# Optimization experiments

Measured on AMD Instinct MI355X. Metric: run time of the kernel, lower is better.

The kernel has to match this reference:

```python
import jax, jax.numpy as jnp
import numpy as np

POOL_RAD = 1.0   # init kwarg pool_rad
N = 16384        # total points
B = 8            # graphs in batch
F = 128          # feature dim
BIG = 1e30

def _voxel_keys(pos, batch, rad):
    # torch_geometric.voxel_grid with start=min-rad/2, end=max+rad/2, batch as extra dim
    start = pos.min(0) - rad * 0.5
    end = pos.max(0) + rad * 0.5
    nv = jnp.floor((end - start) / rad).astype(jnp.int32) + 1  # voxels per spatial dim
    c = jnp.floor((pos - start) / rad).astype(jnp.int32)       # [N,3] voxel coords
    lin = c[:, 0] + c[:, 1] * nv[0] + c[:, 2] * nv[0] * nv[1]
    return lin + batch.astype(jnp.int32) * (nv[0] * nv[1] * nv[2])

def _consecutive(keys, n):
    # consecutive_cluster: relabel to sorted-consecutive ids; perm = last index per cluster
    _, inv = jnp.unique(keys, return_inverse=True, size=n,
                        fill_value=jnp.iinfo(jnp.int32).max)
    inv = inv.reshape(-1)
    perm = jax.ops.segment_max(jnp.arange(n, dtype=jnp.int32), inv, num_segments=n)
    counts = jax.ops.segment_sum(jnp.ones((n,), jnp.int32), inv, num_segments=n)
    return inv, jnp.clip(perm, 0, n - 1), counts

def _nearest(pos, batch, cpos, cbatch, cvalid):
    # nearest centroid within the same graph; invalid/padded centroids masked out
    d = (pos * pos).sum(1)[:, None] - 2.0 * (pos @ cpos.T) + (cpos * cpos).sum(1)[None, :]
    ok = (batch[:, None] == cbatch[None, :]) & cvalid[None, :]
    return jnp.argmin(jnp.where(ok, d, BIG), axis=1)

def _pool(pos, x, batch):
    n = pos.shape[0]
    # stage 1: voxel-grid clustering, centroid positions
    inv1, perm1, cnt1 = _consecutive(_voxel_keys(pos, batch, POOL_RAD), n)
    c1 = jnp.maximum(cnt1, 1).astype(pos.dtype)[:, None]
    cpos = jax.ops.segment_sum(pos, inv1, num_segments=n) / c1
    cbatch = batch[perm1]
    # stage 2: reassign each point to its nearest voxel centroid, relabel
    cl2 = _nearest(jax.lax.stop_gradient(pos), batch,
                   jax.lax.stop_gradient(cpos), cbatch, cnt1 > 0)
    inv2, perm2, cnt2 = _consecutive(cl2, n)
    valid2 = cnt2 > 0
    c2 = jnp.maximum(cnt2, 1).astype(pos.dtype)[:, None]
    pos_out = jax.ops.segment_sum(pos, inv2, num_segments=n) / c2   # mean pos
    x_out = jax.ops.segment_max(x, inv2, num_segments=n)            # aggr='max'
    x_out = jnp.where(valid2[:, None], x_out, 0.0)
    pos_out = jnp.where(valid2[:, None], pos_out, 0.0)
    batch_out = jnp.where(valid2, batch[perm2], -1)
    return x_out, pos_out, batch_out

def setup_inputs():
    key = jax.random.key(0)
    k1, k2 = jax.random.split(key)
    pos = jax.random.uniform(k1, (N, 3), jnp.float32) * 10.0
    x = jax.random.normal(k2, (N, F), jnp.float32)
    batch = jnp.repeat(jnp.arange(B, dtype=jnp.int32), N // B)
    return {"pos": pos, "x": x, "batch": batch}

def reference(pos, x, batch):
    return _pool(pos, x, batch)
```

## Files before the change

kernel.cpp:

```cpp
#include <hip/hip_runtime.h>

#define TPB 256
#define K1SZ 32768

static __device__ __forceinline__ unsigned int fmap(float f) {
  unsigned int b = __float_as_uint(f);
  return (b & 0x80000000u) ? ~b : (b | 0x80000000u);
}
static __device__ __forceinline__ float funmap(unsigned int u) {
  unsigned int b = (u & 0x80000000u) ? (u & 0x7fffffffu) : ~u;
  return __uint_as_float(b);
}

static __device__ __forceinline__ int wave_incl_scan(int v, int lane) {
  #pragma unroll
  for (int off = 1; off < 64; off <<= 1) {
    int u = __shfl_up(v, off);
    if (lane >= off) v += u;
  }
  return v;
}

__global__ void k_init(double* __restrict__ sum1, double* __restrict__ sum2,
                       int* __restrict__ cnt1, int* __restrict__ cnt2,
                       int* __restrict__ perm2, int* __restrict__ flags1,
                       int* __restrict__ flags2, unsigned int* __restrict__ xacc,
                       const float* __restrict__ pos, float* __restrict__ scal,
                       int n, int F) {
  int t = blockIdx.x * blockDim.x + threadIdx.x;
  if (t < n * F) xacc[t] = 0u;
  if (t < 3 * n) { sum1[t] = 0.0; sum2[t] = 0.0; }
  if (t < n) { cnt1[t] = 0; cnt2[t] = 0; perm2[t] = -1; flags2[t] = 0; }
  if (t < K1SZ) flags1[t] = 0;

  if (blockIdx.x == 0) {
    const int tid = threadIdx.x;
    const int lane = tid & 63, wid = tid >> 6;
    float mn[3] = {3.4e38f, 3.4e38f, 3.4e38f};
    float mx[3] = {-3.4e38f, -3.4e38f, -3.4e38f};
    const float4* p4 = (const float4*)pos;
    int np4 = n >> 2;
    for (int j = tid; j < np4; j += TPB) {
      float4 a = p4[3 * j], b = p4[3 * j + 1], c = p4[3 * j + 2];
      mn[0] = fminf(mn[0], fminf(fminf(a.x, a.w), fminf(b.z, c.y)));
      mx[0] = fmaxf(mx[0], fmaxf(fmaxf(a.x, a.w), fmaxf(b.z, c.y)));
      mn[1] = fminf(mn[1], fminf(fminf(a.y, b.x), fminf(b.w, c.z)));
      mx[1] = fmaxf(mx[1], fmaxf(fmaxf(a.y, b.x), fmaxf(b.w, c.z)));
      mn[2] = fminf(mn[2], fminf(fminf(a.z, b.y), fminf(c.x, c.w)));
      mx[2] = fmaxf(mx[2], fmaxf(fmaxf(a.z, b.y), fmaxf(c.x, c.w)));
    }
    if (tid == 0) {
      for (int i = np4 * 4; i < n; ++i)
        for (int d = 0; d < 3; ++d) {
          float v = pos[i * 3 + d];
          mn[d] = fminf(mn[d], v);
          mx[d] = fmaxf(mx[d], v);
        }
    }
    #pragma unroll
    for (int off = 32; off > 0; off >>= 1) {
      #pragma unroll
      for (int d = 0; d < 3; ++d) {
        mn[d] = fminf(mn[d], __shfl_xor(mn[d], off));
        mx[d] = fmaxf(mx[d], __shfl_xor(mx[d], off));
      }
    }
    __shared__ float smn[4][3], smx[4][3];
    if (lane == 0)
      for (int d = 0; d < 3; ++d) { smn[wid][d] = mn[d]; smx[wid][d] = mx[d]; }
    __syncthreads();
    if (tid == 0) {
      float rmn[3], rmx[3];
      for (int d = 0; d < 3; ++d) { rmn[d] = smn[0][d]; rmx[d] = smx[0][d]; }
      for (int w = 1; w < 4; ++w)
        for (int d = 0; d < 3; ++d) {
          rmn[d] = fminf(rmn[d], smn[w][d]);
          rmx[d] = fmaxf(rmx[d], smx[w][d]);
        }
      int nv[3];
      for (int d = 0; d < 3; ++d) {
        float start = rmn[d] - 0.5f;
        float end   = rmx[d] + 0.5f;
        nv[d] = (int)floorf(end - start) + 1;
        scal[d] = start;
      }
      int* isc = (int*)(scal + 3);
      isc[0] = nv[0];
      isc[1] = nv[0] * nv[1];
      isc[2] = nv[0] * nv[1] * nv[2];
      isc[3] = nv[1];
      isc[4] = nv[2];
    }
  }
}

__global__ void k_keys(const float* __restrict__ pos, const int* __restrict__ batch, int n,
                       const float* __restrict__ scal, int* __restrict__ key1,
                       int* __restrict__ flags1) {
  int i = blockIdx.x * blockDim.x + threadIdx.x;
  if (i >= n) return;
  const int* isc = (const int*)(scal + 3);
  int c0 = (int)floorf(pos[i * 3 + 0] - scal[0]);
  int c1 = (int)floorf(pos[i * 3 + 1] - scal[1]);
  int c2 = (int)floorf(pos[i * 3 + 2] - scal[2]);
  int key = c0 + c1 * isc[0] + c2 * isc[1] + batch[i] * isc[2];
  key = min(max(key, 0), K1SZ - 1);
  key1[i] = key;
  flags1[key] = 1;
}

__global__ __launch_bounds__(1024) void k_scan(const int* __restrict__ flags,
                                               int* __restrict__ rank, int L) {
  const int t = threadIdx.x;
  const int lane = t & 63;
  const int wid = t >> 6;
  __shared__ int wsum[16];
  const int4* f4 = (const int4*)flags;
  int4* r4 = (int4*)rank;
  const int n4 = L >> 2;
  int base = 0;
  for (int tile = 0; tile * 1024 < n4; ++tile) {
    int i = tile * 1024 + t;
    int4 v = (i < n4) ? f4[i] : int4{0, 0, 0, 0};
    int q0 = v.x, q1 = q0 + v.y, q2 = q1 + v.z, q3 = q2 + v.w;
    int ws = wave_incl_scan(q3, lane);
    if (lane == 63) wsum[wid] = ws;
    __syncthreads();
    int woff = 0, ttot = 0;
    #pragma unroll
    for (int w = 0; w < 16; ++w) {
      int s = wsum[w];
      if (w < wid) woff += s;
      ttot += s;
    }
    int e = base + woff + (ws - q3);
    if (i < n4) r4[i] = int4{e, e + q0, e + q1, e + q2};
    base += ttot;
    __syncthreads();
  }
}

__global__ void k_assign1(const float* __restrict__ pos, int n,
                          const int* __restrict__ key1, const int* __restrict__ rank1,
                          int* __restrict__ cnt1, double* __restrict__ sum1) {
  int i = blockIdx.x * blockDim.x + threadIdx.x;
  if (i >= n) return;
  int c = rank1[key1[i]];
  atomicAdd(&cnt1[c], 1);
  atomicAdd(&sum1[c * 3 + 0], (double)pos[i * 3 + 0]);
  atomicAdd(&sum1[c * 3 + 1], (double)pos[i * 3 + 1]);
  atomicAdd(&sum1[c * 3 + 2], (double)pos[i * 3 + 2]);
}

__global__ void k_centroid1(int n, const int* __restrict__ cnt1, double* __restrict__ sum1) {
  int k = blockIdx.x * blockDim.x + threadIdx.x;
  if (k >= n) return;
  int c = cnt1[k];
  if (c <= 0) return;
  double inv = 1.0 / (double)c;
  sum1[k * 3 + 0] *= inv;
  sum1[k * 3 + 1] *= inv;
  sum1[k * 3 + 2] *= inv;
}

__global__ void k_nearest(const float* __restrict__ pos, const int* __restrict__ batch, int n,
                          const double* __restrict__ cpos, const int* __restrict__ flags1,
                          const int* __restrict__ rank1, const float* __restrict__ scal,
                          int* __restrict__ cl2, int* __restrict__ flags2) {
  int i = blockIdx.x * blockDim.x + threadIdx.x;
  if (i >= n) return;
  const int* isc = (const int*)(scal + 3);
  const float s0 = scal[0], s1 = scal[1], s2 = scal[2];
  const int nv0 = isc[0], nv01 = isc[1], nvtot = isc[2];
  const int nv1 = isc[3], nv2 = isc[4];
  float pxf = pos[i * 3 + 0], pyf = pos[i * 3 + 1], pzf = pos[i * 3 + 2];
  double px = pxf, py = pyf, pz = pzf;
  int c0 = (int)floorf(pxf - s0);
  int c1 = (int)floorf(pyf - s1);
  int c2 = (int)floorf(pzf - s2);
  int base = batch[i] * nvtot;
  int k0 = min(max(c0 + c1 * nv0 + c2 * nv01 + base, 0), K1SZ - 1);
  int bid = rank1[k0];
  double dx = px - cpos[bid * 3 + 0];
  double dy = py - cpos[bid * 3 + 1];
  double dz = pz - cpos[bid * 3 + 2];
  double best2 = dx * dx + dy * dy + dz * dz;
  for (int oz = -2; oz <= 2; ++oz) {
    int z = c2 + oz;
    if (z < 0 || z >= nv2) continue;
    double lz = (double)s2 + z;
    double gz = fmax(0.0, fmax(lz - pz, pz - (lz + 1.0)));
    double gz2 = gz * gz;
    if (gz2 > best2 + 1e-4) continue;
    for (int oy = -2; oy <= 2; ++oy) {
      int y = c1 + oy;
      if (y < 0 || y >= nv1) continue;
      double ly = (double)s1 + y;
      double gy = fmax(0.0, fmax(ly - py, py - (ly + 1.0)));
      double gzy2 = gz2 + gy * gy;
      if (gzy2 > best2 + 1e-4) continue;
      for (int ox = -2; ox <= 2; ++ox) {
        int xq = c0 + ox;
        if (xq < 0 || xq >= nv0) continue;
        if ((ox | oy | oz) == 0) continue;
        double lx = (double)s0 + xq;
        double gx = fmax(0.0, fmax(lx - px, px - (lx + 1.0)));
        double mind2 = gzy2 + gx * gx;
        if (mind2 > best2 + 1e-4) continue;
        int key = min(xq + y * nv0 + z * nv01 + base, K1SZ - 1);
        if (!flags1[key]) continue;
        int c = rank1[key];
        double ddx = px - cpos[c * 3 + 0];
        double ddy = py - cpos[c * 3 + 1];
        double ddz = pz - cpos[c * 3 + 2];
        double d2 = ddx * ddx + ddy * ddy + ddz * ddz;
        if (d2 < best2 || (d2 == best2 && c < bid)) { best2 = d2; bid = c; }
      }
    }
  }
  cl2[i] = bid;
  flags2[bid] = 1;
}

__global__ void k_assign2_xmax(const float* __restrict__ pos, const float* __restrict__ x,
                               int n, int F, const int* __restrict__ cl2,
                               const int* __restrict__ rank2, int* __restrict__ cnt2,
                               int* __restrict__ perm2, double* __restrict__ sum2,
                               unsigned int* __restrict__ xacc) {
  int t = blockIdx.x * blockDim.x + threadIdx.x;
  if (t >= n * F) return;
  int i = t / F;
  int f = t - i * F;
  int c = rank2[cl2[i]];
  atomicMax(&xacc[c * F + f], fmap(x[t]));
  if (f == 0) {
    atomicAdd(&cnt2[c], 1);
    atomicMax(&perm2[c], i);
    atomicAdd(&sum2[c * 3 + 0], (double)pos[i * 3 + 0]);
    atomicAdd(&sum2[c * 3 + 1], (double)pos[i * 3 + 1]);
    atomicAdd(&sum2[c * 3 + 2], (double)pos[i * 3 + 2]);
  }
}

__global__ void k_finalize(int n, int F, const int* __restrict__ cnt2,
                           const int* __restrict__ perm2, const int* __restrict__ batch,
                           const double* __restrict__ sum2, unsigned int* __restrict__ xacc,
                           float* __restrict__ pos_out, float* __restrict__ batch_out) {
  int t = blockIdx.x * blockDim.x + threadIdx.x;
  if (t < n * F) {
    int j = t / F;
    float out = 0.0f;
    if (cnt2[j] > 0) out = funmap(xacc[t]);
    ((float*)xacc)[t] = out;
  }
  if (t < n) {
    int c = cnt2[t];
    if (c > 0) {
      double inv = 1.0 / (double)c;
      pos_out[t * 3 + 0] = (float)(sum2[t * 3 + 0] * inv);
      pos_out[t * 3 + 1] = (float)(sum2[t * 3 + 1] * inv);
      pos_out[t * 3 + 2] = (float)(sum2[t * 3 + 2] * inv);
      batch_out[t] = (float)batch[perm2[t]];
    } else {
      pos_out[t * 3 + 0] = 0.0f;
      pos_out[t * 3 + 1] = 0.0f;
      pos_out[t * 3 + 2] = 0.0f;
      batch_out[t] = -1.0f;
    }
  }
}

extern "C" void kernel_launch(void* const* d_in, const int* in_sizes, int n_in,
                              void* d_out, int out_size, void* d_ws, size_t ws_size,
                              hipStream_t stream) {
  const float* pos   = (const float*)d_in[0];
  const float* x     = (const float*)d_in[1];
  const int*   batch = (const int*)d_in[2];
  int n = in_sizes[2];
  int F = in_sizes[1] / n;

  char* ws = (char*)d_ws;
  size_t off = 0;
  auto alloc = [&](size_t bytes, size_t align) -> void* {
    off = (off + align - 1) & ~(align - 1);
    void* p = ws + off;
    off += bytes;
    return p;
  };
  double* sum1   = (double*)alloc((size_t)n * 3 * sizeof(double), 16);
  double* sum2   = (double*)alloc((size_t)n * 3 * sizeof(double), 16);
  int* key1      = (int*)alloc((size_t)n * 4, 16);
  int* cl2       = (int*)alloc((size_t)n * 4, 16);
  int* cnt1      = (int*)alloc((size_t)n * 4, 16);
  int* cnt2      = (int*)alloc((size_t)n * 4, 16);
  int* perm2     = (int*)alloc((size_t)n * 4, 16);
  int* flags1    = (int*)alloc((size_t)K1SZ * 4, 16);
  int* rank1     = (int*)alloc((size_t)K1SZ * 4, 16);
  int* flags2    = (int*)alloc((size_t)n * 4, 16);
  int* rank2     = (int*)alloc((size_t)n * 4, 16);
  float* scal    = (float*)alloc(64, 16);

  unsigned int* xacc = (unsigned int*)d_out;
  float* pos_out     = (float*)d_out + (size_t)n * F;
  float* batch_out   = pos_out + (size_t)n * 3;

  int nb  = (n + TPB - 1) / TPB;
  int nbF = (n * F + TPB - 1) / TPB;
  int nbP = (n + 63) / 64;

  k_init<<<nbF, TPB, 0, stream>>>(sum1, sum2, cnt1, cnt2, perm2,
                                  flags1, flags2, xacc, pos, scal, n, F);
  k_keys<<<nb, TPB, 0, stream>>>(pos, batch, n, scal, key1, flags1);
  k_scan<<<1, 1024, 0, stream>>>(flags1, rank1, K1SZ);
  k_assign1<<<nb, TPB, 0, stream>>>(pos, n, key1, rank1, cnt1, sum1);
  k_centroid1<<<nb, TPB, 0, stream>>>(n, cnt1, sum1);
  k_nearest<<<nbP, 64, 0, stream>>>(pos, batch, n, sum1, flags1, rank1, scal, cl2, flags2);
  k_scan<<<1, 1024, 0, stream>>>(flags2, rank2, n);
  k_assign2_xmax<<<nbF, TPB, 0, stream>>>(pos, x, n, F, cl2, rank2, cnt2, perm2,
                                          sum2, xacc);
  k_finalize<<<nbF, TPB, 0, stream>>>(n, F, cnt2, perm2, batch, sum2, xacc,
                                      pos_out, batch_out);
}
```

Measured before the change: 67.15 us.

## Bound scans by active range, fold centroid divide into nearest, vectorize feature passes

The init kernel now also finds the maximum batch id, so the first scan only walks the occupied part of the key space. That scan records the total cluster count, which then bounds how many tiles the second scan processes. The separate centroid-normalisation kernel is removed; k_nearest divides the sums by the counts on the fly. Init, the x max-aggregation and finalize move to float4/uint4 accesses with four atomics per thread. The cost is extra divisions inside the neighbour search, and unwritten rank entries beyond the active range, which are assumed never to be read.

```diff
diff --git a/kernel.cpp b/kernel.cpp
--- a/kernel.cpp
+++ b/kernel.cpp
@@ -24,11 +24,11 @@
 __global__ void k_init(double* __restrict__ sum1, double* __restrict__ sum2,
                        int* __restrict__ cnt1, int* __restrict__ cnt2,
                        int* __restrict__ perm2, int* __restrict__ flags1,
-                       int* __restrict__ flags2, unsigned int* __restrict__ xacc,
-                       const float* __restrict__ pos, float* __restrict__ scal,
-                       int n, int F) {
+                       int* __restrict__ flags2, uint4* __restrict__ xacc4,
+                       const float* __restrict__ pos, const int* __restrict__ batch,
+                       float* __restrict__ scal, int n, int nF4) {
   int t = blockIdx.x * blockDim.x + threadIdx.x;
-  if (t < n * F) xacc[t] = 0u;
+  if (t < nF4) xacc4[t] = uint4{0u, 0u, 0u, 0u};
   if (t < 3 * n) { sum1[t] = 0.0; sum2[t] = 0.0; }
   if (t < n) { cnt1[t] = 0; cnt2[t] = 0; perm2[t] = -1; flags2[t] = 0; }
   if (t < K1SZ) flags1[t] = 0;
@@ -38,7 +38,9 @@
     const int lane = tid & 63, wid = tid >> 6;
     float mn[3] = {3.4e38f, 3.4e38f, 3.4e38f};
     float mx[3] = {-3.4e38f, -3.4e38f, -3.4e38f};
+    int mb = 0;
     const float4* p4 = (const float4*)pos;
+    const int4* b4 = (const int4*)batch;
     int np4 = n >> 2;
     for (int j = tid; j < np4; j += TPB) {
       float4 a = p4[3 * j], b = p4[3 * j + 1], c = p4[3 * j + 2];
@@ -48,14 +50,18 @@
       mx[1] = fmaxf(mx[1], fmaxf(fmaxf(a.y, b.x), fmaxf(b.w, c.z)));
       mn[2] = fminf(mn[2], fminf(fminf(a.z, b.y), fminf(c.x, c.w)));
       mx[2] = fmaxf(mx[2], fmaxf(fmaxf(a.z, b.y), fmaxf(c.x, c.w)));
+      int4 bb = b4[j];
+      mb = max(mb, max(max(bb.x, bb.y), max(bb.z, bb.w)));
     }
     if (tid == 0) {
-      for (int i = np4 * 4; i < n; ++i)
+      for (int i = np4 * 4; i < n; ++i) {
         for (int d = 0; d < 3; ++d) {
           float v = pos[i * 3 + d];
           mn[d] = fminf(mn[d], v);
           mx[d] = fmaxf(mx[d], v);
         }
+        mb = max(mb, batch[i]);
+      }
     }
     #pragma unroll
     for (int off = 32; off > 0; off >>= 1) {
@@ -64,19 +70,26 @@
         mn[d] = fminf(mn[d], __shfl_xor(mn[d], off));
         mx[d] = fmaxf(mx[d], __shfl_xor(mx[d], off));
       }
+      mb = max(mb, __shfl_xor(mb, off));
     }
     __shared__ float smn[4][3], smx[4][3];
-    if (lane == 0)
+    __shared__ int smb[4];
+    if (lane == 0) {
       for (int d = 0; d < 3; ++d) { smn[wid][d] = mn[d]; smx[wid][d] = mx[d]; }
+      smb[wid] = mb;
+    }
     __syncthreads();
     if (tid == 0) {
       float rmn[3], rmx[3];
+      int rmb = smb[0];
       for (int d = 0; d < 3; ++d) { rmn[d] = smn[0][d]; rmx[d] = smx[0][d]; }
-      for (int w = 1; w < 4; ++w)
+      for (int w = 1; w < 4; ++w) {
         for (int d = 0; d < 3; ++d) {
           rmn[d] = fminf(rmn[d], smn[w][d]);
           rmx[d] = fmaxf(rmx[d], smx[w][d]);
         }
+        rmb = max(rmb, smb[w]);
+      }
       int nv[3];
       for (int d = 0; d < 3; ++d) {
         float start = rmn[d] - 0.5f;
@@ -90,6 +103,7 @@
       isc[2] = nv[0] * nv[1] * nv[2];
       isc[3] = nv[1];
       isc[4] = nv[2];
+      isc[5] = rmb + 1;
     }
   }
 }
@@ -109,19 +123,18 @@
   flags1[key] = 1;
 }
 
-__global__ __launch_bounds__(1024) void k_scan(const int* __restrict__ flags,
-                                               int* __restrict__ rank, int L) {
+static __device__ __forceinline__ int scan_body(const int* __restrict__ flags,
+                                                int* __restrict__ rank,
+                                                int ntiles, int n4full, int* wsum) {
   const int t = threadIdx.x;
   const int lane = t & 63;
   const int wid = t >> 6;
-  __shared__ int wsum[16];
   const int4* f4 = (const int4*)flags;
   int4* r4 = (int4*)rank;
-  const int n4 = L >> 2;
   int base = 0;
-  for (int tile = 0; tile * 1024 < n4; ++tile) {
+  for (int tile = 0; tile < ntiles; ++tile) {
     int i = tile * 1024 + t;
-    int4 v = (i < n4) ? f4[i] : int4{0, 0, 0, 0};
+    int4 v = (i < n4full) ? f4[i] : int4{0, 0, 0, 0};
     int q0 = v.x, q1 = q0 + v.y, q2 = q1 + v.z, q3 = q2 + v.w;
     int ws = wave_incl_scan(q3, lane);
     if (lane == 63) wsum[wid] = ws;
@@ -134,10 +147,32 @@
       ttot += s;
     }
     int e = base + woff + (ws - q3);
-    if (i < n4) r4[i] = int4{e, e + q0, e + q1, e + q2};
+    if (i < n4full) r4[i] = int4{e, e + q0, e + q1, e + q2};
     base += ttot;
     __syncthreads();
   }
+  return base;
+}
+
+__global__ __launch_bounds__(1024) void k_scan1(const int* __restrict__ flags,
+                                                int* __restrict__ rank,
+                                                const float* __restrict__ scal) {
+  __shared__ int wsum[16];
+  const int* isc = (const int*)(scal + 3);
+  long long L = (long long)isc[5] * isc[2];
+  int L_eff = (int)(L > K1SZ ? K1SZ : L);
+  int ntiles = (L_eff + 4095) >> 12;
+  int base = scan_body(flags, rank, ntiles, K1SZ >> 2, wsum);
+  if (threadIdx.x == 0) rank[K1SZ] = base;
+}
+
+__global__ __launch_bounds__(1024) void k_scan2(const int* __restrict__ flags,
+                                                int* __restrict__ rank,
+                                                const int* __restrict__ total1, int n) {
+  __shared__ int wsum[16];
+  int L_eff = min(n, *total1);
+  int ntiles = (L_eff + 4095) >> 12;
+  scan_body(flags, rank, ntiles, n >> 2, wsum);
 }
 
 __global__ void k_assign1(const float* __restrict__ pos, int n,
@@ -152,20 +187,10 @@
   atomicAdd(&sum1[c * 3 + 2], (double)pos[i * 3 + 2]);
 }
 
-__global__ void k_centroid1(int n, const int* __restrict__ cnt1, double* __restrict__ sum1) {
-  int k = blockIdx.x * blockDim.x + threadIdx.x;
-  if (k >= n) return;
-  int c = cnt1[k];
-  if (c <= 0) return;
-  double inv = 1.0 / (double)c;
-  sum1[k * 3 + 0] *= inv;
-  sum1[k * 3 + 1] *= inv;
-  sum1[k * 3 + 2] *= inv;
-}
-
 __global__ void k_nearest(const float* __restrict__ pos, const int* __restrict__ batch, int n,
-                          const double* __restrict__ cpos, const int* __restrict__ flags1,
-                          const int* __restrict__ rank1, const float* __restrict__ scal,
+                          const double* __restrict__ sum1, const int* __restrict__ cnt1,
+                          const int* __restrict__ flags1, const int* __restrict__ rank1,
+                          const float* __restrict__ scal,
                           int* __restrict__ cl2, int* __restrict__ flags2) {
   int i = blockIdx.x * blockDim.x + threadIdx.x;
   if (i >= n) return;
@@ -181,40 +206,45 @@
   int base = batch[i] * nvtot;
   int k0 = min(max(c0 + c1 * nv0 + c2 * nv01 + base, 0), K1SZ - 1);
   int bid = rank1[k0];
-  double dx = px - cpos[bid * 3 + 0];
-  double dy = py - cpos[bid * 3 + 1];
-  double dz = pz - cpos[bid * 3 + 2];
-  double best2 = dx * dx + dy * dy + dz * dz;
-  for (int oz = -2; oz <= 2; ++oz) {
-    int z = c2 + oz;
-    if (z < 0 || z >= nv2) continue;
-    double lz = (double)s2 + z;
-    double gz = fmax(0.0, fmax(lz - pz, pz - (lz + 1.0)));
-    double gz2 = gz * gz;
-    if (gz2 > best2 + 1e-4) continue;
-    for (int oy = -2; oy <= 2; ++oy) {
-      int y = c1 + oy;
-      if (y < 0 || y >= nv1) continue;
-      double ly = (double)s1 + y;
-      double gy = fmax(0.0, fmax(ly - py, py - (ly + 1.0)));
-      double gzy2 = gz2 + gy * gy;
-      if (gzy2 > best2 + 1e-4) continue;
-      for (int ox = -2; ox <= 2; ++ox) {
-        int xq = c0 + ox;
-        if (xq < 0 || xq >= nv0) continue;
-        if ((ox | oy | oz) == 0) continue;
-        double lx = (double)s0 + xq;
-        double gx = fmax(0.0, fmax(lx - px, px - (lx + 1.0)));
-        double mind2 = gzy2 + gx * gx;
-        if (mind2 > best2 + 1e-4) continue;
-        int key = min(xq + y * nv0 + z * nv01 + base, K1SZ - 1);
-        if (!flags1[key]) continue;
-        int c = rank1[key];
-        double ddx = px - cpos[c * 3 + 0];
-        double ddy = py - cpos[c * 3 + 1];
-        double ddz = pz - cpos[c * 3 + 2];
-        double d2 = ddx * ddx + ddy * ddy + ddz * ddz;
-        if (d2 < best2 || (d2 == best2 && c < bid)) { best2 = d2; bid = c; }
+  {
+    double inv = 1.0 / (double)cnt1[bid];
+    double dx = px - sum1[bid * 3 + 0] * inv;
+    double dy = py - sum1[bid * 3 + 1] * inv;
+    double dz = pz - sum1[bid * 3 + 2] * inv;
+    double d2 = dx * dx + dy * dy + dz * dz;
+    double best2 = d2;
+    for (int oz = -2; oz <= 2; ++oz) {
+      int z = c2 + oz;
+      if (z < 0 || z >= nv2) continue;
+      double lz = (double)s2 + z;
+      double gz = fmax(0.0, fmax(lz - pz, pz - (lz + 1.0)));
+      double gz2 = gz * gz;
+      if (gz2 > best2 + 1e-4) continue;
+      for (int oy = -2; oy <= 2; ++oy) {
+        int y = c1 + oy;
+        if (y < 0 || y >= nv1) continue;
+        double ly = (double)s1 + y;
+        double gy = fmax(0.0, fmax(ly - py, py - (ly + 1.0)));
+        double gzy2 = gz2 + gy * gy;
+        if (gzy2 > best2 + 1e-4) continue;
+        for (int ox = -2; ox <= 2; ++ox) {
+          int xq = c0 + ox;
+          if (xq < 0 || xq >= nv0) continue;
+          if ((ox | oy | oz) == 0) continue;
+          double lx = (double)s0 + xq;
+          double gx = fmax(0.0, fmax(lx - px, px - (lx + 1.0)));
+          double mind2 = gzy2 + gx * gx;
+          if (mind2 > best2 + 1e-4) continue;
+          int key = min(xq + y * nv0 + z * nv01 + base, K1SZ - 1);
+          if (!flags1[key]) continue;
+          int c = rank1[key];
+          double cinv = 1.0 / (double)cnt1[c];
+          double ddx = px - sum1[c * 3 + 0] * cinv;
+          double ddy = py - sum1[c * 3 + 1] * cinv;
+          double ddz = pz - sum1[c * 3 + 2] * cinv;
+          double dd2 = ddx * ddx + ddy * ddy + ddz * ddz;
+          if (dd2 < best2 || (dd2 == best2 && c < bid)) { best2 = dd2; bid = c; }
+        }
       }
     }
   }
@@ -222,18 +252,23 @@
   flags2[bid] = 1;
 }
 
-__global__ void k_assign2_xmax(const float* __restrict__ pos, const float* __restrict__ x,
-                               int n, int F, const int* __restrict__ cl2,
+__global__ void k_assign2_xmax(const float* __restrict__ pos, const float4* __restrict__ x4,
+                               int n, int F4, int F, const int* __restrict__ cl2,
                                const int* __restrict__ rank2, int* __restrict__ cnt2,
                                int* __restrict__ perm2, double* __restrict__ sum2,
                                unsigned int* __restrict__ xacc) {
   int t = blockIdx.x * blockDim.x + threadIdx.x;
-  if (t >= n * F) return;
-  int i = t / F;
-  int f = t - i * F;
+  if (t >= n * F4) return;
+  int i = t / F4;
+  int q = t - i * F4;
   int c = rank2[cl2[i]];
-  atomicMax(&xacc[c * F + f], fmap(x[t]));
-  if (f == 0) {
+  float4 v = x4[t];
+  unsigned int* dst = &xacc[c * F + q * 4];
+  atomicMax(dst + 0, fmap(v.x));
+  atomicMax(dst + 1, fmap(v.y));
+  atomicMax(dst + 2, fmap(v.z));
+  atomicMax(dst + 3, fmap(v.w));
+  if (q == 0) {
     atomicAdd(&cnt2[c], 1);
     atomicMax(&perm2[c], i);
     atomicAdd(&sum2[c * 3 + 0], (double)pos[i * 3 + 0]);
@@ -242,16 +277,19 @@
   }
 }
 
-__global__ void k_finalize(int n, int F, const int* __restrict__ cnt2,
+__global__ void k_finalize(int n, int F4, const int* __restrict__ cnt2,
                            const int* __restrict__ perm2, const int* __restrict__ batch,
-                           const double* __restrict__ sum2, unsigned int* __restrict__ xacc,
+                           const double* __restrict__ sum2, uint4* __restrict__ xacc4,
                            float* __restrict__ pos_out, float* __restrict__ batch_out) {
   int t = blockIdx.x * blockDim.x + threadIdx.x;
-  if (t < n * F) {
-    int j = t / F;
-    float out = 0.0f;
-    if (cnt2[j] > 0) out = funmap(xacc[t]);
-    ((float*)xacc)[t] = out;
+  if (t < n * F4) {
+    int j = t / F4;
+    float4 o = {0.0f, 0.0f, 0.0f, 0.0f};
+    if (cnt2[j] > 0) {
+      uint4 v = xacc4[t];
+      o.x = funmap(v.x); o.y = funmap(v.y); o.z = funmap(v.z); o.w = funmap(v.w);
+    }
+    ((float4*)xacc4)[t] = o;
   }
   if (t < n) {
     int c = cnt2[t];
@@ -278,6 +316,8 @@
   const int*   batch = (const int*)d_in[2];
   int n = in_sizes[2];
   int F = in_sizes[1] / n;
+  int F4 = F >> 2;
+  int nF4 = n * F4;
 
   char* ws = (char*)d_ws;
   size_t off = 0;
@@ -295,7 +335,7 @@
   int* cnt2      = (int*)alloc((size_t)n * 4, 16);
   int* perm2     = (int*)alloc((size_t)n * 4, 16);
   int* flags1    = (int*)alloc((size_t)K1SZ * 4, 16);
-  int* rank1     = (int*)alloc((size_t)K1SZ * 4, 16);
+  int* rank1     = (int*)alloc(((size_t)K1SZ + 4) * 4, 16);
   int* flags2    = (int*)alloc((size_t)n * 4, 16);
   int* rank2     = (int*)alloc((size_t)n * 4, 16);
   float* scal    = (float*)alloc(64, 16);
@@ -304,20 +344,20 @@
   float* pos_out     = (float*)d_out + (size_t)n * F;
   float* batch_out   = pos_out + (size_t)n * 3;
 
-  int nb  = (n + TPB - 1) / TPB;
-  int nbF = (n * F + TPB - 1) / TPB;
-  int nbP = (n + 63) / 64;
-
-  k_init<<<nbF, TPB, 0, stream>>>(sum1, sum2, cnt1, cnt2, perm2,
-                                  flags1, flags2, xacc, pos, scal, n, F);
+  int nb   = (n + TPB - 1) / TPB;
+  int nbV  = (nF4 + TPB - 1) / TPB;
+  int nbP  = (n + 63) / 64;
+
+  k_init<<<nbV, TPB, 0, stream>>>(sum1, sum2, cnt1, cnt2, perm2, flags1, flags2,
+                                  (uint4*)xacc, pos, batch, scal, n, nF4);
   k_keys<<<nb, TPB, 0, stream>>>(pos, batch, n, scal, key1, flags1);
-  k_scan<<<1, 1024, 0, stream>>>(flags1, rank1, K1SZ);
+  k_scan1<<<1, 1024, 0, stream>>>(flags1, rank1, scal);
   k_assign1<<<nb, TPB, 0, stream>>>(pos, n, key1, rank1, cnt1, sum1);
-  k_centroid1<<<nb, TPB, 0, stream>>>(n, cnt1, sum1);
-  k_nearest<<<nbP, 64, 0, stream>>>(pos, batch, n, sum1, flags1, rank1, scal, cl2, flags2);
-  k_scan<<<1, 1024, 0, stream>>>(flags2, rank2, n);
-  k_assign2_xmax<<<nbF, TPB, 0, stream>>>(pos, x, n, F, cl2, rank2, cnt2, perm2,
-                                          sum2, xacc);
-  k_finalize<<<nbF, TPB, 0, stream>>>(n, F, cnt2, perm2, batch, sum2, xacc,
-                                      pos_out, batch_out);
-}
+  k_nearest<<<nbP, 64, 0, stream>>>(pos, batch, n, sum1, cnt1, flags1, rank1, scal,
+                                    cl2, flags2);
+  k_scan2<<<1, 1024, 0, stream>>>(flags2, rank2, rank1 + K1SZ, n);
+  k_assign2_xmax<<<nbV, TPB, 0, stream>>>(pos, (const float4*)x, n, F4, F, cl2, rank2,
+                                          cnt2, perm2, sum2, xacc);
+  k_finalize<<<nbV, TPB, 0, stream>>>(n, F4, cnt2, perm2, batch, sum2,
+                                      (uint4*)xacc, pos_out, batch_out);
+}
```

New measurement: 72.60 us. 8.1% more time.
